# Kernel optimization log

Hardware: AMD Instinct MI355X
Metric: run time of the kernel (lower is better)

The kernel has to match this reference:

```python
import jax, jax.numpy as jnp
import numpy as np

B, S, D, H = 4, 2048, 1024, 16
HD = D // H  # head dim = 64


def setup_inputs() -> dict:
    key = jax.random.key(0)
    ks = jax.random.split(key, 11)
    sc = 1.0 / np.sqrt(D)
    return {
        "q": jax.random.normal(ks[0], (B, S, D), jnp.float32),
        "k": jax.random.normal(ks[1], (B, S, D), jnp.float32),
        "v": jax.random.normal(ks[2], (B, S, D), jnp.float32),
        "w_q": jax.random.normal(ks[3], (D, D), jnp.float32) * sc,
        "b_q": jnp.zeros((D,), jnp.float32),
        "w_k": jax.random.normal(ks[4], (D, D), jnp.float32) * sc,
        "b_k": jnp.zeros((D,), jnp.float32),
        "w_v": jax.random.normal(ks[5], (D, D), jnp.float32) * sc,
        "b_v": jnp.zeros((D,), jnp.float32),
        "w_fc": jax.random.normal(ks[6], (D, D), jnp.float32) * sc,
        "b_fc": jnp.zeros((D,), jnp.float32),
    }


def reference(q, k, v, w_q, b_q, w_k, b_k, w_v, b_v, w_fc, b_fc):
    scale = jnp.asarray(np.sqrt(HD), q.dtype)
    # QKV projections: [B,S,D] @ [D,D]^T (torch Linear: x @ W^T + b)
    Q = (q @ w_q.T + b_q).reshape(B, S, H, HD).transpose(0, 2, 1, 3)  # [B,H,S,HD]
    K = (k @ w_k.T + b_k).reshape(B, S, H, HD).transpose(0, 2, 1, 3)
    V = (v @ w_v.T + b_v).reshape(B, S, H, HD).transpose(0, 2, 1, 3)
    energy = jnp.einsum('bhqd,bhkd->bhqk', Q, K) / scale  # [B,H,S,S]
    attn = jax.nn.softmax(energy, axis=-1)  # dropout is identity in eval / p=0
    x = jnp.einsum('bhqk,bhkd->bhqd', attn, V)  # [B,H,S,HD]
    x = x.transpose(0, 2, 1, 3).reshape(B, S, D)
    return x @ w_fc.T + b_fc
```

## Files before the change

### kernel.cpp

```cpp
#include <hip/hip_runtime.h>
#include <stdint.h>

#define BN 4
#define SEQ 2048
#define DM 1024
#define NH 16
#define HD 64
#define ROWS (BN*SEQ)

typedef float  f32x4  __attribute__((ext_vector_type(4)));
typedef __bf16 bf16x8 __attribute__((ext_vector_type(8)));
typedef __bf16 bf16x4 __attribute__((ext_vector_type(4)));

#define QSCALE 0.18033688f

__device__ inline bf16x8 cvt8(const float* __restrict__ src) {
    float4 x0 = *(const float4*)src;
    float4 x1 = *(const float4*)(src + 4);
    bf16x8 r;
    r[0] = (__bf16)x0.x; r[1] = (__bf16)x0.y; r[2] = (__bf16)x0.z; r[3] = (__bf16)x0.w;
    r[4] = (__bf16)x1.x; r[5] = (__bf16)x1.y; r[6] = (__bf16)x1.z; r[7] = (__bf16)x1.w;
    return r;
}

__device__ inline void gl_lds16(const void* g, void* l) {
    __builtin_amdgcn_global_load_lds((const __attribute__((address_space(1))) uint32_t*)g,
                                     (__attribute__((address_space(3))) uint32_t*)l, 16, 0, 0);
}

__global__ __launch_bounds__(256) void cast3(
    const float* __restrict__ a0, const float* __restrict__ a1, const float* __restrict__ a2,
    __bf16* __restrict__ o0, __bf16* __restrict__ o1, __bf16* __restrict__ o2, int n8) {
    int t = blockIdx.x * 256 + threadIdx.x;
    if (t >= n8) return;
    const float* in = (blockIdx.y == 0) ? a0 : (blockIdx.y == 1) ? a1 : a2;
    __bf16* out     = (blockIdx.y == 0) ? o0 : (blockIdx.y == 1) ? o1 : o2;
    *(bf16x8*)&out[(size_t)t * 8] = cvt8(&in[(size_t)t * 8]);
}

__global__ __launch_bounds__(256) void cast4(
    const float* __restrict__ a0, const float* __restrict__ a1,
    const float* __restrict__ a2, const float* __restrict__ a3,
    __bf16* __restrict__ o0, __bf16* __restrict__ o1,
    __bf16* __restrict__ o2, __bf16* __restrict__ o3, int n8) {
    int t = blockIdx.x * 256 + threadIdx.x;
    if (t >= n8) return;
    const float* in = (blockIdx.y == 0) ? a0 : (blockIdx.y == 1) ? a1 : (blockIdx.y == 2) ? a2 : a3;
    __bf16* out     = (blockIdx.y == 0) ? o0 : (blockIdx.y == 1) ? o1 : (blockIdx.y == 2) ? o2 : o3;
    *(bf16x8*)&out[(size_t)t * 8] = cvt8(&in[(size_t)t * 8]);
}

#define GEMM_CORE_GLDS(Xp, Wp)                                                     \
    __shared__ __align__(16) __bf16 As[128 * 32];                                  \
    __shared__ __align__(16) __bf16 Bs[128 * 32];                                  \
    const int tid  = threadIdx.x;                                                  \
    const int lane = tid & 63;                                                     \
    const int wave = tid >> 6;                                                     \
    const int wm = (wave >> 1) * 64;                                               \
    const int wn = (wave & 1) * 64;                                                \
    const int c16 = lane & 15;                                                     \
    const int g8  = (lane >> 4) * 8;                                               \
    const int row0 = blockIdx.x * 128;                                             \
    const int col0 = blockIdx.y * 128;                                             \
    f32x4 acc[4][4] = {};                                                          \
    for (int k0 = 0; k0 < DM; k0 += 32) {                                          \
        __syncthreads();                                                           \
        _Pragma("unroll")                                                          \
        for (int h = 0; h < 2; h++) {                                              \
            int cidx = h * 256 + tid;                                              \
            gl_lds16(&Xp[(size_t)(row0 + (cidx >> 2)) * DM + k0 + (cidx & 3) * 8], \
                     &As[(size_t)(h * 256 + wave * 64) * 8]);                      \
            gl_lds16(&Wp[(size_t)(col0 + (cidx >> 2)) * DM + k0 + (cidx & 3) * 8], \
                     &Bs[(size_t)(h * 256 + wave * 64) * 8]);                      \
        }                                                                          \
        __syncthreads();                                                           \
        bf16x8 a[4], bfr[4];                                                       \
        _Pragma("unroll")                                                          \
        for (int i = 0; i < 4; i++) a[i]   = *(const bf16x8*)&As[(wm + i * 16 + c16) * 32 + g8]; \
        _Pragma("unroll")                                                          \
        for (int i = 0; i < 4; i++) bfr[i] = *(const bf16x8*)&Bs[(wn + i * 16 + c16) * 32 + g8]; \
        _Pragma("unroll")                                                          \
        for (int mi = 0; mi < 4; mi++)                                             \
            _Pragma("unroll")                                                      \
            for (int ni = 0; ni < 4; ni++)                                         \
                acc[mi][ni] = __builtin_amdgcn_mfma_f32_16x16x32_bf16(a[mi], bfr[ni], acc[mi][ni], 0, 0, 0); \
    }

__global__ __launch_bounds__(256) void gemm_qk_f(
    const __bf16* __restrict__ qb, const __bf16* __restrict__ kb,
    const __bf16* __restrict__ wqb, const __bf16* __restrict__ wkb,
    const float* __restrict__ bq, const float* __restrict__ bk,
    __bf16* __restrict__ Qp, __bf16* __restrict__ Kp)
{
    const int z = blockIdx.z;
    const __bf16* X = z ? kb : qb;
    const __bf16* W = z ? wkb : wqb;
    const float* bias = z ? bk : bq;
    __bf16* O = z ? Kp : Qp;
    const float qsc = z ? 1.0f : QSCALE;

    GEMM_CORE_GLDS(X, W)

    #pragma unroll
    for (int mi = 0; mi < 4; mi++) {
        int r0 = row0 + wm + mi * 16 + (lane >> 4) * 4;
        #pragma unroll
        for (int ni = 0; ni < 4; ni++) {
            int col = col0 + wn + ni * 16 + c16;
            float bsv = bias[col];
            int h = col >> 6, d = col & 63;
            #pragma unroll
            for (int i = 0; i < 4; i++) {
                int r = r0 + i; int b = r >> 11, s = r & 2047;
                O[((size_t)(b * NH + h) * SEQ + s) * HD + d] = (__bf16)((acc[mi][ni][i] + bsv) * qsc);
            }
        }
    }
}

__global__ __launch_bounds__(256) void gemm_v_f(
    const __bf16* __restrict__ vb, const __bf16* __restrict__ wvb,
    const float* __restrict__ bv, __bf16* __restrict__ Vt)
{
    GEMM_CORE_GLDS(vb, wvb)

    #pragma unroll
    for (int mi = 0; mi < 4; mi++) {
        int r0 = row0 + wm + mi * 16 + (lane >> 4) * 4;
        #pragma unroll
        for (int ni = 0; ni < 4; ni++) {
            int col = col0 + wn + ni * 16 + c16;
            float bsv = bv[col];
            int h = col >> 6, d = col & 63;
            int b = r0 >> 11, s0 = r0 & 2047;
            size_t base = ((size_t)((b * NH + h) * HD + d)) * SEQ + s0;
            #pragma unroll
            for (int i = 0; i < 4; i++)
                Vt[base + i] = (__bf16)(acc[mi][ni][i] + bsv);
        }
    }
}

__global__ __launch_bounds__(256) void gemm_fc_f(
    const __bf16* __restrict__ Xc, const __bf16* __restrict__ Wfb,
    const float* __restrict__ bias, float* __restrict__ out)
{
    GEMM_CORE_GLDS(Xc, Wfb)

    #pragma unroll
    for (int mi = 0; mi < 4; mi++) {
        int r0 = row0 + wm + mi * 16 + (lane >> 4) * 4;
        #pragma unroll
        for (int ni = 0; ni < 4; ni++) {
            int col = col0 + wn + ni * 16 + c16;
            float bsv = bias[col];
            #pragma unroll
            for (int i = 0; i < 4; i++)
                out[(size_t)(r0 + i) * DM + col] = acc[mi][ni][i] + bsv;
        }
    }
}

__global__ __launch_bounds__(256) void gemm_qk(
    const __bf16* __restrict__ qb, const __bf16* __restrict__ kb,
    const float* __restrict__ wqf, const float* __restrict__ wkf,
    const float* __restrict__ bq, const float* __restrict__ bk,
    __bf16* __restrict__ Qp, __bf16* __restrict__ Kp)
{
    const int z = blockIdx.z;
    const __bf16* X = z ? kb : qb;
    const float* W  = z ? wkf : wqf;
    const float* bias = z ? bk : bq;
    __bf16* O = z ? Kp : Qp;
    const float qsc = z ? 1.0f : QSCALE;

    __shared__ __align__(16) __bf16 As[128 * 32];
    __shared__ __align__(16) __bf16 Bs[128 * 32];

    const int tid  = threadIdx.x;
    const int lane = tid & 63;
    const int wave = tid >> 6;
    const int wm = (wave >> 1) * 64;
    const int wn = (wave & 1) * 64;
    const int c16 = lane & 15;
    const int g8  = (lane >> 4) * 8;
    const int row0 = blockIdx.x * 128;
    const int col0 = blockIdx.y * 128;
    const int brow = tid >> 1;
    const int bcc  = (tid & 1) * 16;

    f32x4 acc[4][4] = {};
    for (int k0 = 0; k0 < DM; k0 += 32) {
        __syncthreads();
        #pragma unroll
        for (int h = 0; h < 2; h++) {
            int cidx = h * 256 + tid;
            gl_lds16(&X[(size_t)(row0 + (cidx >> 2)) * DM + k0 + (cidx & 3) * 8],
                     &As[(size_t)(h * 256 + wave * 64) * 8]);
        }
        *(bf16x8*)&Bs[brow * 32 + bcc]     = cvt8(&W[(size_t)(col0 + brow) * DM + k0 + bcc]);
        *(bf16x8*)&Bs[brow * 32 + bcc + 8] = cvt8(&W[(size_t)(col0 + brow) * DM + k0 + bcc + 8]);
        __syncthreads();

        bf16x8 a[4], bfr[4];
        #pragma unroll
        for (int i = 0; i < 4; i++) a[i]   = *(const bf16x8*)&As[(wm + i * 16 + c16) * 32 + g8];
        #pragma unroll
        for (int i = 0; i < 4; i++) bfr[i] = *(const bf16x8*)&Bs[(wn + i * 16 + c16) * 32 + g8];
        #pragma unroll
        for (int mi = 0; mi < 4; mi++)
            #pragma unroll
            for (int ni = 0; ni < 4; ni++)
                acc[mi][ni] = __builtin_amdgcn_mfma_f32_16x16x32_bf16(a[mi], bfr[ni], acc[mi][ni], 0, 0, 0);
    }

    #pragma unroll
    for (int mi = 0; mi < 4; mi++) {
        int r0 = row0 + wm + mi * 16 + (lane >> 4) * 4;
        #pragma unroll
        for (int ni = 0; ni < 4; ni++) {
            int col = col0 + wn + ni * 16 + c16;
            float bsv = bias[col];
            int h = col >> 6, d = col & 63;
            #pragma unroll
            for (int i = 0; i < 4; i++) {
                int r = r0 + i; int b = r >> 11, s = r & 2047;
                O[((size_t)(b * NH + h) * SEQ + s) * HD + d] = (__bf16)((acc[mi][ni][i] + bsv) * qsc);
            }
        }
    }
}

__global__ __launch_bounds__(256) void gemm_v(
    const float* __restrict__ vf, const float* __restrict__ wvf,
    const float* __restrict__ bv, __bf16* __restrict__ Vt)
{
    __shared__ __align__(16) __bf16 As[128 * 32];
    __shared__ __align__(16) __bf16 Bs[128 * 32];

    const int tid  = threadIdx.x;
    const int lane = tid & 63;
    const int wave = tid >> 6;
    const int wm = (wave >> 1) * 64;
    const int wn = (wave & 1) * 64;
    const int c16 = lane & 15;
    const int g8  = (lane >> 4) * 8;
    const int row0 = blockIdx.x * 128;
    const int col0 = blockIdx.y * 128;
    const int brow = tid >> 1;
    const int bcc  = (tid & 1) * 16;

    f32x4 acc[4][4] = {};
    for (int k0 = 0; k0 < DM; k0 += 32) {
        __syncthreads();
        *(bf16x8*)&As[brow * 32 + bcc]     = cvt8(&vf[(size_t)(row0 + brow) * DM + k0 + bcc]);
        *(bf16x8*)&As[brow * 32 + bcc + 8] = cvt8(&vf[(size_t)(row0 + brow) * DM + k0 + bcc + 8]);
        *(bf16x8*)&Bs[brow * 32 + bcc]     = cvt8(&wvf[(size_t)(col0 + brow) * DM + k0 + bcc]);
        *(bf16x8*)&Bs[brow * 32 + bcc + 8] = cvt8(&wvf[(size_t)(col0 + brow) * DM + k0 + bcc + 8]);
        __syncthreads();

        bf16x8 a[4], bfr[4];
        #pragma unroll
        for (int i = 0; i < 4; i++) a[i]   = *(const bf16x8*)&As[(wm + i * 16 + c16) * 32 + g8];
        #pragma unroll
        for (int i = 0; i < 4; i++) bfr[i] = *(const bf16x8*)&Bs[(wn + i * 16 + c16) * 32 + g8];
        #pragma unroll
        for (int mi = 0; mi < 4; mi++)
            #pragma unroll
            for (int ni = 0; ni < 4; ni++)
                acc[mi][ni] = __builtin_amdgcn_mfma_f32_16x16x32_bf16(a[mi], bfr[ni], acc[mi][ni], 0, 0, 0);
    }

    #pragma unroll
    for (int mi = 0; mi < 4; mi++) {
        int r0 = row0 + wm + mi * 16 + (lane >> 4) * 4;
        #pragma unroll
        for (int ni = 0; ni < 4; ni++) {
            int col = col0 + wn + ni * 16 + c16;
            float bsv = bv[col];
            int h = col >> 6, d = col & 63;
            int b = r0 >> 11, s0 = r0 & 2047;
            size_t base = ((size_t)((b * NH + h) * HD + d)) * SEQ + s0;
            #pragma unroll
            for (int i = 0; i < 4; i++)
                Vt[base + i] = (__bf16)(acc[mi][ni][i] + bsv);
        }
    }
}

__global__ __launch_bounds__(256) void gemm_fc(
    const __bf16* __restrict__ Xc, const float* __restrict__ Wf,
    const float* __restrict__ bias, float* __restrict__ out)
{
    __shared__ __align__(16) __bf16 As[128 * 32];
    __shared__ __align__(16) __bf16 Bs[128 * 32];

    const int tid  = threadIdx.x;
    const int lane = tid & 63;
    const int wave = tid >> 6;
    const int wm = (wave >> 1) * 64;
    const int wn = (wave & 1) * 64;
    const int c16 = lane & 15;
    const int g8  = (lane >> 4) * 8;
    const int row0 = blockIdx.x * 128;
    const int col0 = blockIdx.y * 128;
    const int brow = tid >> 1;
    const int bcc  = (tid & 1) * 16;

    f32x4 acc[4][4] = {};
    for (int k0 = 0; k0 < DM; k0 += 32) {
        __syncthreads();
        #pragma unroll
        for (int h = 0; h < 2; h++) {
            int cidx = h * 256 + tid;
            gl_lds16(&Xc[(size_t)(row0 + (cidx >> 2)) * DM + k0 + (cidx & 3) * 8],
                     &As[(size_t)(h * 256 + wave * 64) * 8]);
        }
        *(bf16x8*)&Bs[brow * 32 + bcc]     = cvt8(&Wf[(size_t)(col0 + brow) * DM + k0 + bcc]);
        *(bf16x8*)&Bs[brow * 32 + bcc + 8] = cvt8(&Wf[(size_t)(col0 + brow) * DM + k0 + bcc + 8]);
        __syncthreads();

        bf16x8 a[4], bfr[4];
        #pragma unroll
        for (int i = 0; i < 4; i++) a[i]   = *(const bf16x8*)&As[(wm + i * 16 + c16) * 32 + g8];
        #pragma unroll
        for (int i = 0; i < 4; i++) bfr[i] = *(const bf16x8*)&Bs[(wn + i * 16 + c16) * 32 + g8];
        #pragma unroll
        for (int mi = 0; mi < 4; mi++)
            #pragma unroll
            for (int ni = 0; ni < 4; ni++)
                acc[mi][ni] = __builtin_amdgcn_mfma_f32_16x16x32_bf16(a[mi], bfr[ni], acc[mi][ni], 0, 0, 0);
    }

    #pragma unroll
    for (int mi = 0; mi < 4; mi++) {
        int r0 = row0 + wm + mi * 16 + (lane >> 4) * 4;
        #pragma unroll
        for (int ni = 0; ni < 4; ni++) {
            int col = col0 + wn + ni * 16 + c16;
            float bsv = bias[col];
            #pragma unroll
            for (int i = 0; i < 4; i++)
                out[(size_t)(r0 + i) * DM + col] = acc[mi][ni][i] + bsv;
        }
    }
}

__global__ __launch_bounds__(256, 4) void attn_kernel(
    const __bf16* __restrict__ Qp, const __bf16* __restrict__ Kp,
    const __bf16* __restrict__ Vt, __bf16* __restrict__ ctx)
{
    __shared__ __align__(16) __bf16 Ks[64 * 64];
    __shared__ __align__(16) __bf16 Vs[64 * 64];
    __shared__ __align__(16) __bf16 Ps[4][32 * 64];

    const int tid  = threadIdx.x;
    const int lane = tid & 63;
    const int w    = tid >> 6;
    const int bh   = blockIdx.x;
    const int q0   = blockIdx.y * 128 + w * 32;

    const __bf16* Qb = Qp + (size_t)bh * SEQ * HD;
    const __bf16* Kb = Kp + (size_t)bh * SEQ * HD;
    const __bf16* Vb = Vt + (size_t)bh * HD * SEQ;

    const int c16 = lane & 15;
    const int g   = lane >> 4;
    const int sw  = c16 & 7;

    bf16x8 qf[2][2];
    #pragma unroll
    for (int qs = 0; qs < 2; qs++)
        #pragma unroll
        for (int kc = 0; kc < 2; kc++)
            qf[qs][kc] = *(const bf16x8*)&Qb[(size_t)(q0 + qs * 16 + c16) * HD + kc * 32 + g * 8];

    float lp[2] = {0.f, 0.f};
    f32x4 o[4][2] = {};

    const int srow = (w * 16) + (lane >> 3);
    const int sj   = (lane & 7) ^ (lane >> 3);

    for (int kt = 0; kt < SEQ / 64; kt++) {
        const int k0 = kt * 64;
        __syncthreads();
        #pragma unroll
        for (int h = 0; h < 2; h++) {
            int r = srow + h * 8;
            gl_lds16(&Kb[(size_t)(k0 + r) * HD + sj * 8], &Ks[(size_t)(w * 16 + h * 8) * 64]);
            gl_lds16(&Vb[(size_t)r * SEQ + k0 + sj * 8],  &Vs[(size_t)(w * 16 + h * 8) * 64]);
        }
        __syncthreads();

        f32x4 sc[4][2] = {};
        #pragma unroll
        for (int t = 0; t < 4; t++) {
            #pragma unroll
            for (int kc = 0; kc < 2; kc++) {
                bf16x8 kf = *(const bf16x8*)&Ks[(t * 16 + c16) * 64 + ((kc * 4 + g) ^ sw) * 8];
                sc[t][0] = __builtin_amdgcn_mfma_f32_16x16x32_bf16(kf, qf[0][kc], sc[t][0], 0, 0, 0);
                sc[t][1] = __builtin_amdgcn_mfma_f32_16x16x32_bf16(kf, qf[1][kc], sc[t][1], 0, 0, 0);
            }
        }

        #pragma unroll
        for (int qs = 0; qs < 2; qs++) {
            float ps = 0.f;
            #pragma unroll
            for (int t = 0; t < 4; t++) {
                bf16x4 pk;
                #pragma unroll
                for (int i = 0; i < 4; i++) {
                    float pv = exp2f(sc[t][qs][i]);
                    ps += pv;
                    pk[i] = (__bf16)pv;
                }
                *(bf16x4*)&Ps[w][(qs * 16 + c16) * 64 + ((2 * t + (g >> 1)) ^ sw) * 8 + (g & 1) * 4] = pk;
            }
            lp[qs] += ps;
        }

        bf16x8 pf[2][2];
        #pragma unroll
        for (int qs = 0; qs < 2; qs++)
            #pragma unroll
            for (int kc = 0; kc < 2; kc++)
                pf[qs][kc] = *(const bf16x8*)&Ps[w][(qs * 16 + c16) * 64 + ((kc * 4 + g) ^ sw) * 8];

        #pragma unroll
        for (int t = 0; t < 4; t++) {
            #pragma unroll
            for (int kc = 0; kc < 2; kc++) {
                bf16x8 vfr = *(const bf16x8*)&Vs[(t * 16 + c16) * 64 + ((kc * 4 + g) ^ sw) * 8];
                o[t][0] = __builtin_amdgcn_mfma_f32_16x16x32_bf16(vfr, pf[0][kc], o[t][0], 0, 0, 0);
                o[t][1] = __builtin_amdgcn_mfma_f32_16x16x32_bf16(vfr, pf[1][kc], o[t][1], 0, 0, 0);
            }
        }
    }

    const int hh = bh & (NH - 1);
    const int bb = bh >> 4;
    #pragma unroll
    for (int qs = 0; qs < 2; qs++) {
        float l = lp[qs];
        l += __shfl_xor(l, 16, 64);
        l += __shfl_xor(l, 32, 64);
        float inv = 1.f / l;
        int s = q0 + qs * 16 + c16;
        #pragma unroll
        for (int t = 0; t < 4; t++) {
            bf16x4 ov;
            #pragma unroll
            for (int i = 0; i < 4; i++) ov[i] = (__bf16)(o[t][qs][i] * inv);
            *(bf16x4*)&ctx[((size_t)(bb * SEQ + s)) * DM + hh * HD + t * 16 + g * 4] = ov;
        }
    }
}

extern "C" void kernel_launch(void* const* d_in, const int* in_sizes, int n_in,
                              void* d_out, int out_size, void* d_ws, size_t ws_size,
                              hipStream_t stream) {
    const float* q    = (const float*)d_in[0];
    const float* k    = (const float*)d_in[1];
    const float* v    = (const float*)d_in[2];
    const float* w_q  = (const float*)d_in[3];
    const float* b_q  = (const float*)d_in[4];
    const float* w_k  = (const float*)d_in[5];
    const float* b_k  = (const float*)d_in[6];
    const float* w_v  = (const float*)d_in[7];
    const float* b_v  = (const float*)d_in[8];
    const float* w_fc = (const float*)d_in[9];
    const float* b_fc = (const float*)d_in[10];
    float* out = (float*)d_out;

    __bf16* qb = (__bf16*)d_out;
    __bf16* kb = qb + (size_t)ROWS * DM;

    char* p = (char*)d_ws;
    auto alloc = [&](size_t bytes) { char* r = p; p += (bytes + 255) & ~(size_t)255; return r; };
    const size_t XSZ = (size_t)ROWS * DM * 2;
    const size_t WSZ = (size_t)DM * DM * 2;

    __bf16* Qp  = (__bf16*)alloc(XSZ);
    __bf16* Kp  = (__bf16*)alloc(XSZ);
    __bf16* Vt  = (__bf16*)alloc(XSZ);
    __bf16* ctx = (__bf16*)alloc(XSZ);

    const size_t base_need = (size_t)(p - (char*)d_ws);
    const size_t fast_need = base_need + 4 * (WSZ + 256);

    const int n8x = ROWS * DM / 8;
    const int n8w = DM * DM / 8;

    __bf16* vb = Qp;

    cast3<<<dim3(n8x / 256, 3), 256, 0, stream>>>(q, k, v, qb, kb, vb, n8x);

    if (ws_size >= fast_need) {
        __bf16* wqb  = (__bf16*)alloc(WSZ);
        __bf16* wkb  = (__bf16*)alloc(WSZ);
        __bf16* wvb  = (__bf16*)alloc(WSZ);
        __bf16* wfcb = (__bf16*)alloc(WSZ);

        cast4<<<dim3(n8w / 256, 4), 256, 0, stream>>>(
            w_q, w_k, w_v, w_fc, wqb, wkb, wvb, wfcb, n8w);

        gemm_v_f<<<dim3(ROWS / 128, DM / 128), 256, 0, stream>>>(vb, wvb, b_v, Vt);
        gemm_qk_f<<<dim3(ROWS / 128, DM / 128, 2), 256, 0, stream>>>(
            qb, kb, wqb, wkb, b_q, b_k, Qp, Kp);

        attn_kernel<<<dim3(BN * NH, SEQ / 128), 256, 0, stream>>>(Qp, Kp, Vt, ctx);

        gemm_fc_f<<<dim3(ROWS / 128, DM / 128), 256, 0, stream>>>(ctx, wfcb, b_fc, out);
    } else {
        gemm_v<<<dim3(ROWS / 128, DM / 128), 256, 0, stream>>>(v, w_v, b_v, Vt);
        gemm_qk<<<dim3(ROWS / 128, DM / 128, 2), 256, 0, stream>>>(
            qb, kb, w_q, w_k, b_q, b_k, Qp, Kp);

        attn_kernel<<<dim3(BN * NH, SEQ / 128), 256, 0, stream>>>(Qp, Kp, Vt, ctx);

        gemm_fc<<<dim3(ROWS / 128, DM / 128), 256, 0, stream>>>(ctx, w_fc, b_fc, out);
    }
}
```

Baseline: 361.4 us.

## Merge Q/K/V projection GEMMs into one launch and shrink attention blocks

Fuses the separate V and QK projection kernels into a single gemm_qkv_f launch with a three-way grid z dimension, and moves the bf16 V staging buffer to the ctx buffer so it no longer aliases Qp. The attention kernel is halved to 2 waves (128 threads, 64 query rows per block), doubling the grid and having each wave load twice as many K/V rows into shared memory. This aims to cut launch overhead and fill the GPU better in attention, at the cost of loading K/V tiles once per 64 query rows instead of per 128.

New measurement: 391.1 us. 1.08x slower.

```diff
diff --git a/kernel.cpp b/kernel.cpp
--- a/kernel.cpp
+++ b/kernel.cpp
@@ -86,57 +86,55 @@
                 acc[mi][ni] = __builtin_amdgcn_mfma_f32_16x16x32_bf16(a[mi], bfr[ni], acc[mi][ni], 0, 0, 0); \
     }
 
-__global__ __launch_bounds__(256) void gemm_qk_f(
+__global__ __launch_bounds__(256) void gemm_qkv_f(
     const __bf16* __restrict__ qb, const __bf16* __restrict__ kb,
+    const __bf16* __restrict__ vb,
     const __bf16* __restrict__ wqb, const __bf16* __restrict__ wkb,
+    const __bf16* __restrict__ wvb,
     const float* __restrict__ bq, const float* __restrict__ bk,
-    __bf16* __restrict__ Qp, __bf16* __restrict__ Kp)
+    const float* __restrict__ bv,
+    __bf16* __restrict__ Qp, __bf16* __restrict__ Kp, __bf16* __restrict__ Vt)
 {
     const int z = blockIdx.z;
-    const __bf16* X = z ? kb : qb;
-    const __bf16* W = z ? wkb : wqb;
-    const float* bias = z ? bk : bq;
-    __bf16* O = z ? Kp : Qp;
-    const float qsc = z ? 1.0f : QSCALE;
+    const __bf16* X = (z == 0) ? qb : (z == 1) ? kb : vb;
+    const __bf16* W = (z == 0) ? wqb : (z == 1) ? wkb : wvb;
+    const float* bias = (z == 0) ? bq : (z == 1) ? bk : bv;
 
     GEMM_CORE_GLDS(X, W)
 
-    #pragma unroll
-    for (int mi = 0; mi < 4; mi++) {
-        int r0 = row0 + wm + mi * 16 + (lane >> 4) * 4;
-        #pragma unroll
-        for (int ni = 0; ni < 4; ni++) {
-            int col = col0 + wn + ni * 16 + c16;
-            float bsv = bias[col];
-            int h = col >> 6, d = col & 63;
-            #pragma unroll
-            for (int i = 0; i < 4; i++) {
-                int r = r0 + i; int b = r >> 11, s = r & 2047;
-                O[((size_t)(b * NH + h) * SEQ + s) * HD + d] = (__bf16)((acc[mi][ni][i] + bsv) * qsc);
+    if (z < 2) {
+        __bf16* O = z ? Kp : Qp;
+        const float qsc = z ? 1.0f : QSCALE;
+        #pragma unroll
+        for (int mi = 0; mi < 4; mi++) {
+            int r0 = row0 + wm + mi * 16 + (lane >> 4) * 4;
+            #pragma unroll
+            for (int ni = 0; ni < 4; ni++) {
+                int col = col0 + wn + ni * 16 + c16;
+                float bsv = bias[col];
+                int h = col >> 6, d = col & 63;
+                #pragma unroll
+                for (int i = 0; i < 4; i++) {
+                    int r = r0 + i; int b = r >> 11, s = r & 2047;
+                    O[((size_t)(b * NH + h) * SEQ + s) * HD + d] = (__bf16)((acc[mi][ni][i] + bsv) * qsc);
+                }
             }
         }
-    }
-}
-
-__global__ __launch_bounds__(256) void gemm_v_f(
-    const __bf16* __restrict__ vb, const __bf16* __restrict__ wvb,
-    const float* __restrict__ bv, __bf16* __restrict__ Vt)
-{
-    GEMM_CORE_GLDS(vb, wvb)
-
-    #pragma unroll
-    for (int mi = 0; mi < 4; mi++) {
-        int r0 = row0 + wm + mi * 16 + (lane >> 4) * 4;
-        #pragma unroll
-        for (int ni = 0; ni < 4; ni++) {
-            int col = col0 + wn + ni * 16 + c16;
-            float bsv = bv[col];
-            int h = col >> 6, d = col & 63;
-            int b = r0 >> 11, s0 = r0 & 2047;
-            size_t base = ((size_t)((b * NH + h) * HD + d)) * SEQ + s0;
-            #pragma unroll
-            for (int i = 0; i < 4; i++)
-                Vt[base + i] = (__bf16)(acc[mi][ni][i] + bsv);
+    } else {
+        #pragma unroll
+        for (int mi = 0; mi < 4; mi++) {
+            int r0 = row0 + wm + mi * 16 + (lane >> 4) * 4;
+            #pragma unroll
+            for (int ni = 0; ni < 4; ni++) {
+                int col = col0 + wn + ni * 16 + c16;
+                float bsv = bias[col];
+                int h = col >> 6, d = col & 63;
+                int b = r0 >> 11, s0 = r0 & 2047;
+                size_t base = ((size_t)((b * NH + h) * HD + d)) * SEQ + s0;
+                #pragma unroll
+                for (int i = 0; i < 4; i++)
+                    Vt[base + i] = (__bf16)(acc[mi][ni][i] + bsv);
+            }
         }
     }
 }
@@ -346,19 +344,19 @@
     }
 }
 
-__global__ __launch_bounds__(256, 4) void attn_kernel(
+__global__ __launch_bounds__(128) void attn_kernel(
     const __bf16* __restrict__ Qp, const __bf16* __restrict__ Kp,
     const __bf16* __restrict__ Vt, __bf16* __restrict__ ctx)
 {
     __shared__ __align__(16) __bf16 Ks[64 * 64];
     __shared__ __align__(16) __bf16 Vs[64 * 64];
-    __shared__ __align__(16) __bf16 Ps[4][32 * 64];
+    __shared__ __align__(16) __bf16 Ps[2][32 * 64];
 
     const int tid  = threadIdx.x;
     const int lane = tid & 63;
     const int w    = tid >> 6;
     const int bh   = blockIdx.x;
-    const int q0   = blockIdx.y * 128 + w * 32;
+    const int q0   = blockIdx.y * 64 + w * 32;
 
     const __bf16* Qb = Qp + (size_t)bh * SEQ * HD;
     const __bf16* Kb = Kp + (size_t)bh * SEQ * HD;
@@ -378,17 +376,17 @@
     float lp[2] = {0.f, 0.f};
     f32x4 o[4][2] = {};
 
-    const int srow = (w * 16) + (lane >> 3);
+    const int srow = (w * 32) + (lane >> 3);
     const int sj   = (lane & 7) ^ (lane >> 3);
 
     for (int kt = 0; kt < SEQ / 64; kt++) {
         const int k0 = kt * 64;
         __syncthreads();
         #pragma unroll
-        for (int h = 0; h < 2; h++) {
+        for (int h = 0; h < 4; h++) {
             int r = srow + h * 8;
-            gl_lds16(&Kb[(size_t)(k0 + r) * HD + sj * 8], &Ks[(size_t)(w * 16 + h * 8) * 64]);
-            gl_lds16(&Vb[(size_t)r * SEQ + k0 + sj * 8],  &Vs[(size_t)(w * 16 + h * 8) * 64]);
+            gl_lds16(&Kb[(size_t)(k0 + r) * HD + sj * 8], &Ks[(size_t)(w * 32 + h * 8) * 64]);
+            gl_lds16(&Vb[(size_t)r * SEQ + k0 + sj * 8],  &Vs[(size_t)(w * 32 + h * 8) * 64]);
         }
         __syncthreads();
 
@@ -492,7 +490,7 @@
     const int n8x = ROWS * DM / 8;
     const int n8w = DM * DM / 8;
 
-    __bf16* vb = Qp;
+    __bf16* vb = ctx;
 
     cast3<<<dim3(n8x / 256, 3), 256, 0, stream>>>(q, k, v, qb, kb, vb, n8x);
 
@@ -505,11 +503,10 @@
         cast4<<<dim3(n8w / 256, 4), 256, 0, stream>>>(
             w_q, w_k, w_v, w_fc, wqb, wkb, wvb, wfcb, n8w);
 
-        gemm_v_f<<<dim3(ROWS / 128, DM / 128), 256, 0, stream>>>(vb, wvb, b_v, Vt);
-        gemm_qk_f<<<dim3(ROWS / 128, DM / 128, 2), 256, 0, stream>>>(
-            qb, kb, wqb, wkb, b_q, b_k, Qp, Kp);
-
-        attn_kernel<<<dim3(BN * NH, SEQ / 128), 256, 0, stream>>>(Qp, Kp, Vt, ctx);
+        gemm_qkv_f<<<dim3(ROWS / 128, DM / 128, 3), 256, 0, stream>>>(
+            qb, kb, vb, wqb, wkb, wvb, b_q, b_k, b_v, Qp, Kp, Vt);
+
+        attn_kernel<<<dim3(BN * NH, SEQ / 64), 128, 0, stream>>>(Qp, Kp, Vt, ctx);
 
         gemm_fc_f<<<dim3(ROWS / 128, DM / 128), 256, 0, stream>>>(ctx, wfcb, b_fc, out);
     } else {
@@ -517,7 +514,7 @@
         gemm_qk<<<dim3(ROWS / 128, DM / 128, 2), 256, 0, stream>>>(
             qb, kb, w_q, w_k, b_q, b_k, Qp, Kp);
 
-        attn_kernel<<<dim3(BN * NH, SEQ / 128), 256, 0, stream>>>(Qp, Kp, Vt, ctx);
+        attn_kernel<<<dim3(BN * NH, SEQ / 64), 128, 0, stream>>>(Qp, Kp, Vt, ctx);
 
         gemm_fc<<<dim3(ROWS / 128, DM / 128), 256, 0, stream>>>(ctx, w_fc, b_fc, out);
     }
```
